# Performance work log

Hardware: AMD Instinct MI355X
Metric: run time of the kernel (lower is better)

Reference implementation:

```python
import jax, jax.numpy as jnp
import numpy as np

B, L, H = 2, 64, 64
VOCAB = 32000
HEADS = 8
HPH = H // HEADS  # harmonics per head


def setup_inputs() -> dict:
    key = jax.random.key(0)
    ks = jax.random.split(key, 6)
    freqs = jax.random.normal(ks[0], (B, L, H), dtype=jnp.float32)
    amps = jax.random.normal(ks[1], (B, L, H), dtype=jnp.float32)
    phases = jax.random.normal(ks[2], (B, L, H), dtype=jnp.float32)
    vocab_patterns = jax.random.normal(ks[3], (VOCAB, HEADS, HPH), dtype=jnp.float32)
    # nn.Parameter init is zeros; use small noise so gradients/paths are nontrivial
    interference_phases = 0.1 * jax.random.normal(ks[4], (HEADS, HPH), dtype=jnp.float32)
    # nn.Linear(num_heads, 1): weight (1, heads), bias (1,)
    W = jax.random.normal(ks[5], (1, HEADS), dtype=jnp.float32) / np.sqrt(HEADS)
    b = jnp.zeros((1,), dtype=jnp.float32)
    return {"freqs": freqs, "amps": amps, "phases": phases,
            "vocab_patterns": vocab_patterns,
            "interference_phases": interference_phases,
            "W": W, "b": b}


def reference(freqs, amps, phases, vocab_patterns, interference_phases, W, b):
    Bb, Ll, Hh = freqs.shape
    heads = vocab_patterns.shape[1]
    hph = Hh // heads
    f = freqs.reshape(Bb, Ll, heads, hph)
    a = amps.reshape(Bb, Ll, heads, hph)
    p = phases.reshape(Bb, Ll, heads, hph)
    # phase_alignment has no vocab dependence: fold amp * cos(phase diff) first
    c = a * jnp.cos(p - interference_phases[None, None, :, :])  # (B,L,heads,hph)
    scores = []
    for h in range(heads):  # small fixed loop over heads (avoids (B,L,heads,V,hph) blowup)
        f_h = f[:, :, h, :]                      # (B,L,hph)
        vf = vocab_patterns[:, h, :]             # (V,hph)
        fm = jnp.exp(-jnp.abs(f_h[:, :, None, :] - vf[None, None, :, :]))  # (B,L,V,hph)
        scores.append(jnp.einsum('blk,blvk->blv', c[:, :, h, :], fm))
    s = jnp.stack(scores, axis=-1)               # (B,L,V,heads)
    logits = jnp.einsum('blvh,oh->blvo', s, W)[..., 0] + b[0]  # (B,L,V)
    return logits
```

## Files before the change

### kernel.cpp

```cpp
#include <hip/hip_runtime.h>
#include <math.h>

#define VOCAB   32000
#define BLTOT   128
#define HTOT    64
#define BLT     8
#define VPB     256

#define LOG2E   1.44269504088896340736f

typedef float v2f __attribute__((ext_vector_type(2)));

static __device__ __forceinline__ v2f pk_add(v2f a, v2f b) {
    v2f d;
    asm("v_pk_add_f32 %0, %1, %2" : "=v"(d) : "v"(a), "v"(b));
    return d;
}
static __device__ __forceinline__ v2f pk_fma(v2f a, v2f b, v2f c) {
    asm("v_pk_fma_f32 %0, %1, %2, %0" : "+v"(c) : "v"(a), "v"(b));
    return c;
}

__global__ void prep_kernel(const float* __restrict__ freqs,
                            const float* __restrict__ amps,
                            const float* __restrict__ phases,
                            const float* __restrict__ ip,
                            const float* __restrict__ W,
                            float* __restrict__ ws) {
    int t = blockIdx.x * blockDim.x + threadIdx.x;
    if (t >= BLTOT * HTOT) return;
    int bl = t >> 6;
    int j  = t & 63;
    float negfe = -freqs[t] * LOG2E;
    float cw = amps[t] * cosf(phases[t] - ip[j]) * W[j >> 3];
    int jj = j >> 2, u = j & 3;
    float* base = ws + bl * 128 + jj * 8;
    base[u]     = negfe;
    base[4 + u] = cw;
}

__global__ __launch_bounds__(VPB, 6) void
wave_main(const float* __restrict__ vp,
          const float* __restrict__ uni,
          const float* __restrict__ bptr,
          float* __restrict__ out) {
    const int v   = blockIdx.x * VPB + threadIdx.x;
    const int bl0 = blockIdx.y * BLT;

    __shared__ float4 smem[BLT * 16 * 2];

    smem[threadIdx.x] = ((const float4*)(uni + bl0 * 128))[threadIdx.x];
    __syncthreads();

    const float4* __restrict__ vp4 = (const float4*)vp;

    v2f acc01[BLT], acc23[BLT];
#pragma unroll
    for (int i = 0; i < BLT; ++i) { acc01[i] = (v2f)(0.0f); acc23[i] = (v2f)(0.0f); }

#pragma unroll 2
    for (int jj = 0; jj < 16; ++jj) {
        const float4 vf = vp4[v * 16 + jj];
        v2f ve01, ve23;
        ve01.x = vf.x * LOG2E; ve01.y = vf.y * LOG2E;
        ve23.x = vf.z * LOG2E; ve23.y = vf.w * LOG2E;
#pragma unroll
        for (int i = 0; i < BLT; ++i) {
            const float4 f4 = smem[(i * 16 + jj) * 2];
            const float4 c4 = smem[(i * 16 + jj) * 2 + 1];
            v2f d01 = pk_add(v2f{f4.x, f4.y}, ve01);
            v2f d23 = pk_add(v2f{f4.z, f4.w}, ve23);
            v2f e01, e23;
            e01.x = __builtin_amdgcn_exp2f(-__builtin_fabsf(d01.x));
            e01.y = __builtin_amdgcn_exp2f(-__builtin_fabsf(d01.y));
            e23.x = __builtin_amdgcn_exp2f(-__builtin_fabsf(d23.x));
            e23.y = __builtin_amdgcn_exp2f(-__builtin_fabsf(d23.y));
            acc01[i] = pk_fma(v2f{c4.x, c4.y}, e01, acc01[i]);
            acc23[i] = pk_fma(v2f{c4.z, c4.w}, e23, acc23[i]);
        }
    }

    const float b0 = bptr[0];
#pragma unroll
    for (int i = 0; i < BLT; ++i) {
        float s = (acc01[i].x + acc01[i].y) + (acc23[i].x + acc23[i].y);
        out[(bl0 + i) * VOCAB + v] = s + b0;
    }
}

extern "C" void kernel_launch(void* const* d_in, const int* in_sizes, int n_in,
                              void* d_out, int out_size, void* d_ws, size_t ws_size,
                              hipStream_t stream) {
    const float* freqs  = (const float*)d_in[0];
    const float* amps   = (const float*)d_in[1];
    const float* phases = (const float*)d_in[2];
    const float* vp     = (const float*)d_in[3];
    const float* ip     = (const float*)d_in[4];
    const float* W      = (const float*)d_in[5];
    const float* b      = (const float*)d_in[6];
    float* out = (float*)d_out;
    float* ws  = (float*)d_ws;

    prep_kernel<<<dim3(32), dim3(256), 0, stream>>>(freqs, amps, phases, ip, W, ws);

    wave_main<<<dim3(VOCAB / VPB, BLTOT / BLT), dim3(VPB), 0, stream>>>(vp, ws, b, out);
}
```

Measured before the change: 122.5 us.

## Register-tile four vocab entries per thread and halve BL rows per block

```diff
diff --git a/kernel.cpp b/kernel.cpp
--- a/kernel.cpp
+++ b/kernel.cpp
@@ -4,8 +4,9 @@
 #define VOCAB   32000
 #define BLTOT   128
 #define HTOT    64
-#define BLT     8
-#define VPB     256
+#define BLT     4
+#define VPB     320
+#define VT      4
 
 #define LOG2E   1.44269504088896340736f
 
@@ -39,53 +40,65 @@
     base[4 + u] = cw;
 }
 
-__global__ __launch_bounds__(VPB, 6) void
+__global__ __launch_bounds__(VPB, 4) void
 wave_main(const float* __restrict__ vp,
           const float* __restrict__ uni,
           const float* __restrict__ bptr,
           float* __restrict__ out) {
-    const int v   = blockIdx.x * VPB + threadIdx.x;
+    const int v0  = blockIdx.x * (VPB * VT) + threadIdx.x;
     const int bl0 = blockIdx.y * BLT;
 
     __shared__ float4 smem[BLT * 16 * 2];
-
-    smem[threadIdx.x] = ((const float4*)(uni + bl0 * 128))[threadIdx.x];
+    if (threadIdx.x < BLT * 16 * 2)
+        smem[threadIdx.x] = ((const float4*)(uni + bl0 * 128))[threadIdx.x];
     __syncthreads();
 
     const float4* __restrict__ vp4 = (const float4*)vp;
 
-    v2f acc01[BLT], acc23[BLT];
+    v2f acc01[BLT][VT], acc23[BLT][VT];
 #pragma unroll
-    for (int i = 0; i < BLT; ++i) { acc01[i] = (v2f)(0.0f); acc23[i] = (v2f)(0.0f); }
+    for (int i = 0; i < BLT; ++i)
+#pragma unroll
+        for (int k = 0; k < VT; ++k) { acc01[i][k] = (v2f)(0.0f); acc23[i][k] = (v2f)(0.0f); }
 
 #pragma unroll 2
     for (int jj = 0; jj < 16; ++jj) {
-        const float4 vf = vp4[v * 16 + jj];
-        v2f ve01, ve23;
-        ve01.x = vf.x * LOG2E; ve01.y = vf.y * LOG2E;
-        ve23.x = vf.z * LOG2E; ve23.y = vf.w * LOG2E;
+        v2f ve01[VT], ve23[VT];
+#pragma unroll
+        for (int k = 0; k < VT; ++k) {
+            const float4 vf = vp4[(v0 + k * VPB) * 16 + jj];
+            ve01[k].x = vf.x * LOG2E; ve01[k].y = vf.y * LOG2E;
+            ve23[k].x = vf.z * LOG2E; ve23[k].y = vf.w * LOG2E;
+        }
 #pragma unroll
         for (int i = 0; i < BLT; ++i) {
             const float4 f4 = smem[(i * 16 + jj) * 2];
             const float4 c4 = smem[(i * 16 + jj) * 2 + 1];
-            v2f d01 = pk_add(v2f{f4.x, f4.y}, ve01);
-            v2f d23 = pk_add(v2f{f4.z, f4.w}, ve23);
-            v2f e01, e23;
-            e01.x = __builtin_amdgcn_exp2f(-__builtin_fabsf(d01.x));
-            e01.y = __builtin_amdgcn_exp2f(-__builtin_fabsf(d01.y));
-            e23.x = __builtin_amdgcn_exp2f(-__builtin_fabsf(d23.x));
-            e23.y = __builtin_amdgcn_exp2f(-__builtin_fabsf(d23.y));
-            acc01[i] = pk_fma(v2f{c4.x, c4.y}, e01, acc01[i]);
-            acc23[i] = pk_fma(v2f{c4.z, c4.w}, e23, acc23[i]);
+            const v2f f01 = {f4.x, f4.y}, f23 = {f4.z, f4.w};
+            const v2f c01 = {c4.x, c4.y}, c23 = {c4.z, c4.w};
+#pragma unroll
+            for (int k = 0; k < VT; ++k) {
+                v2f d01 = pk_add(f01, ve01[k]);
+                v2f d23 = pk_add(f23, ve23[k]);
+                v2f e01, e23;
+                e01.x = __builtin_amdgcn_exp2f(-__builtin_fabsf(d01.x));
+                e01.y = __builtin_amdgcn_exp2f(-__builtin_fabsf(d01.y));
+                e23.x = __builtin_amdgcn_exp2f(-__builtin_fabsf(d23.x));
+                e23.y = __builtin_amdgcn_exp2f(-__builtin_fabsf(d23.y));
+                acc01[i][k] = pk_fma(c01, e01, acc01[i][k]);
+                acc23[i][k] = pk_fma(c23, e23, acc23[i][k]);
+            }
         }
     }
 
     const float b0 = bptr[0];
 #pragma unroll
-    for (int i = 0; i < BLT; ++i) {
-        float s = (acc01[i].x + acc01[i].y) + (acc23[i].x + acc23[i].y);
-        out[(bl0 + i) * VOCAB + v] = s + b0;
-    }
+    for (int i = 0; i < BLT; ++i)
+#pragma unroll
+        for (int k = 0; k < VT; ++k) {
+            float s = (acc01[i][k].x + acc01[i][k].y) + (acc23[i][k].x + acc23[i][k].y);
+            out[(bl0 + i) * VOCAB + v0 + k * VPB] = s + b0;
+        }
 }
 
 extern "C" void kernel_launch(void* const* d_in, const int* in_sizes, int n_in,
@@ -103,5 +116,5 @@
 
     prep_kernel<<<dim3(32), dim3(256), 0, stream>>>(freqs, amps, phases, ip, W, ws);
 
-    wave_main<<<dim3(VOCAB / VPB, BLTOT / BLT), dim3(VPB), 0, stream>>>(vp, ws, b, out);
+    wave_main<<<dim3(VOCAB / (VPB * VT), BLTOT / BLT), dim3(VPB), 0, stream>>>(vp, ws, b, out);
 }
```

Result: slower. 150.5 us (+22.8%).

## Replace per-element exp(-|f-v|) with min of precomputed exponential products

Applied to the files above, without the earlier changes.

```diff
diff --git a/kernel.cpp b/kernel.cpp
--- a/kernel.cpp
+++ b/kernel.cpp
@@ -11,9 +11,9 @@
 
 typedef float v2f __attribute__((ext_vector_type(2)));
 
-static __device__ __forceinline__ v2f pk_add(v2f a, v2f b) {
+static __device__ __forceinline__ v2f pk_mul(v2f a, v2f b) {
     v2f d;
-    asm("v_pk_add_f32 %0, %1, %2" : "=v"(d) : "v"(a), "v"(b));
+    asm("v_pk_mul_f32 %0, %1, %2" : "=v"(d) : "v"(a), "v"(b));
     return d;
 }
 static __device__ __forceinline__ v2f pk_fma(v2f a, v2f b, v2f c) {
@@ -31,25 +31,32 @@
     if (t >= BLTOT * HTOT) return;
     int bl = t >> 6;
     int j  = t & 63;
-    float negfe = -freqs[t] * LOG2E;
+    float fe = freqs[t] * LOG2E;
     float cw = amps[t] * cosf(phases[t] - ip[j]) * W[j >> 3];
     int jj = j >> 2, u = j & 3;
-    float* base = ws + bl * 128 + jj * 8;
-    base[u]     = negfe;
-    base[4 + u] = cw;
+    float* base = ws + bl * 192 + jj * 12;
+    base[u]     = __builtin_amdgcn_exp2f(fe);
+    base[4 + u] = __builtin_amdgcn_exp2f(-fe);
+    base[8 + u] = cw;
 }
 
-__global__ __launch_bounds__(VPB, 6) void
+__global__ __launch_bounds__(VPB, 4) void
 wave_main(const float* __restrict__ vp,
           const float* __restrict__ uni,
           const float* __restrict__ bptr,
           float* __restrict__ out) {
-    const int v   = blockIdx.x * VPB + threadIdx.x;
+    const int tid = threadIdx.x;
+    const int v   = blockIdx.x * VPB + tid;
     const int bl0 = blockIdx.y * BLT;
 
-    __shared__ float4 smem[BLT * 16 * 2];
+    __shared__ float4 smem[BLT * 16 * 3];
 
-    smem[threadIdx.x] = ((const float4*)(uni + bl0 * 128))[threadIdx.x];
+    {
+        const float4* src4 = (const float4*)(uni + bl0 * 192);
+#pragma unroll
+        for (int s = tid; s < BLT * 16 * 3; s += VPB)
+            smem[s] = src4[s];
+    }
     __syncthreads();
 
     const float4* __restrict__ vp4 = (const float4*)vp;
@@ -61,22 +68,30 @@
 #pragma unroll 2
     for (int jj = 0; jj < 16; ++jj) {
         const float4 vf = vp4[v * 16 + jj];
-        v2f ve01, ve23;
-        ve01.x = vf.x * LOG2E; ve01.y = vf.y * LOG2E;
-        ve23.x = vf.z * LOG2E; ve23.y = vf.w * LOG2E;
+        v2f ev01, ev23, emv01, emv23;
+        {
+            float ax = vf.x * LOG2E, ay = vf.y * LOG2E;
+            float az = vf.z * LOG2E, aw = vf.w * LOG2E;
+            ev01.x  = __builtin_amdgcn_exp2f( ax);  emv01.x = __builtin_amdgcn_exp2f(-ax);
+            ev01.y  = __builtin_amdgcn_exp2f( ay);  emv01.y = __builtin_amdgcn_exp2f(-ay);
+            ev23.x  = __builtin_amdgcn_exp2f( az);  emv23.x = __builtin_amdgcn_exp2f(-az);
+            ev23.y  = __builtin_amdgcn_exp2f( aw);  emv23.y = __builtin_amdgcn_exp2f(-aw);
+        }
 #pragma unroll
         for (int i = 0; i < BLT; ++i) {
-            const float4 f4 = smem[(i * 16 + jj) * 2];
-            const float4 c4 = smem[(i * 16 + jj) * 2 + 1];
-            v2f d01 = pk_add(v2f{f4.x, f4.y}, ve01);
-            v2f d23 = pk_add(v2f{f4.z, f4.w}, ve23);
-            v2f e01, e23;
-            e01.x = __builtin_amdgcn_exp2f(-__builtin_fabsf(d01.x));
-            e01.y = __builtin_amdgcn_exp2f(-__builtin_fabsf(d01.y));
-            e23.x = __builtin_amdgcn_exp2f(-__builtin_fabsf(d23.x));
-            e23.y = __builtin_amdgcn_exp2f(-__builtin_fabsf(d23.y));
-            acc01[i] = pk_fma(v2f{c4.x, c4.y}, e01, acc01[i]);
-            acc23[i] = pk_fma(v2f{c4.z, c4.w}, e23, acc23[i]);
+            const int base = (i * 16 + jj) * 3;
+            const float4 ef4  = smem[base];
+            const float4 emf4 = smem[base + 1];
+            const float4 cw4  = smem[base + 2];
+            v2f t1 = pk_mul(v2f{ef4.x,  ef4.y},  emv01);
+            v2f t2 = pk_mul(v2f{emf4.x, emf4.y}, ev01);
+            v2f t3 = pk_mul(v2f{ef4.z,  ef4.w},  emv23);
+            v2f t4 = pk_mul(v2f{emf4.z, emf4.w}, ev23);
+            v2f m01, m23;
+            m01.x = fminf(t1.x, t2.x);  m01.y = fminf(t1.y, t2.y);
+            m23.x = fminf(t3.x, t4.x);  m23.y = fminf(t3.y, t4.y);
+            acc01[i] = pk_fma(v2f{cw4.x, cw4.y}, m01, acc01[i]);
+            acc23[i] = pk_fma(v2f{cw4.z, cw4.w}, m23, acc23[i]);
         }
     }
 
```

Measured after the change: 164.4 us. 1.34x slower.
